# Kernel optimization log

Hardware: AMD Instinct MI355X
Metric: run time of the kernel (lower is better)

## Reference

```python
import jax, jax.numpy as jnp
import numpy as np

B, N, DIM, INTER, HEAD = 2, 2048, 1024, 1024, 16
N_SEG = 4


def setup_inputs() -> dict:
    key = jax.random.key(0)
    k0, k1, k2, k3 = jax.random.split(key, 4)
    features = jax.random.normal(k0, (B, N, DIM), dtype=jnp.float32)
    mask = jax.random.randint(k1, (B, N, N), 0, N_SEG, dtype=jnp.int32)
    W_qkv = jax.random.normal(k2, (DIM, 3 * INTER), dtype=jnp.float32) * 0.02
    W_out = jax.random.normal(k3, (INTER, DIM), dtype=jnp.float32) * 0.02
    return {"features": features, "mask": mask, "W_qkv": W_qkv, "W_out": W_out,
            "n_segments": N_SEG}


def reference(features, mask, W_qkv, W_out, n_segments):
    b, n, dim = features.shape
    h = HEAD
    scale = INTER ** (-0.5)  # NOTE: original scales by inter_dim, not per-head dim
    qkv = features @ W_qkv                              # [b, n, 3*inter]
    q, k, v = jnp.split(qkv, 3, axis=-1)
    q = q.reshape(b, n, h, -1)                          # [b, n, h, d]
    k = k.reshape(b, n, h, -1)
    v = v.reshape(b, n, h, -1)
    alpha = jnp.einsum('bihd,bjhd->bhij', q, k) * scale  # [b, h, n, n]
    exps = jnp.exp(alpha)
    out = jnp.zeros((b, n, h, v.shape[-1]), dtype=features.dtype)
    # loop over fixed small segment-id set; ids absent from mask contribute 0,
    # exactly matching the torch.unique loop in the original.
    for seg in range(n_segments):
        m = (mask == seg)[:, None, :, :]                # [b, 1, n, n] -> broadcast over h
        fe = jnp.where(m, exps, 0.0)
        s = jnp.sum(fe, axis=-1, keepdims=True)
        att = fe / jnp.where(s == 0, 1.0, s)            # masked softmax (no max-shift, faithful)
        out = out + jnp.einsum('bhij,bjhd->bihd', att, v)
    out = out.reshape(b, n, h * v.shape[-1])            # [b, n, inter]
    return out @ W_out                                  # dropout at eval = identity
```

## Files before the change

### kernel.cpp

```cpp
#include <hip/hip_runtime.h>
#include <hip/hip_bf16.h>

#define BB 2
#define NN 2048
#define DIM 1024
#define INTER 1024
#define NHEAD 16
#define HDIM 64
#define NSEG 4
#define QKVW (3 * INTER)

typedef __attribute__((ext_vector_type(8))) short bf16x8;
typedef __attribute__((ext_vector_type(4))) float f32x4;

static __device__ __forceinline__ unsigned short f2bf(float f) {
    __hip_bfloat16 h = __float2bfloat16(f);
    return *reinterpret_cast<unsigned short*>(&h);
}
static __device__ __forceinline__ float bf2f(unsigned short u) {
    unsigned int x = ((unsigned int)u) << 16;
    return __builtin_bit_cast(float, x);
}
static __device__ __forceinline__ unsigned int pack_bf16_rne(float lo, float hi) {
    unsigned int u = __builtin_bit_cast(unsigned int, lo);
    unsigned int v = __builtin_bit_cast(unsigned int, hi);
    u += 0x7FFFu + ((u >> 16) & 1u);
    v += 0x7FFFu + ((v >> 16) & 1u);
    return (u >> 16) | (v & 0xFFFF0000u);
}

__global__ __launch_bounds__(256) void conv_f32_bf16(const float* __restrict__ in,
                                                     unsigned short* __restrict__ out) {
    int i = (blockIdx.x * 256 + threadIdx.x) * 4;
    float4 v = *(const float4*)&in[i];
    ushort4 o = {f2bf(v.x), f2bf(v.y), f2bf(v.z), f2bf(v.w)};
    *(ushort4*)&out[i] = o;
}

__global__ __launch_bounds__(256) void transp_f32_bf16(const float* __restrict__ in,
                                                       unsigned short* __restrict__ out,
                                                       int R, int C) {
    __shared__ float tile[64][65];
    const int r0 = blockIdx.y * 64, c0 = blockIdx.x * 64;
    const int t = threadIdx.x;
#pragma unroll
    for (int it = 0; it < 4; ++it) {
        int r = it * 16 + (t >> 4);
        int c = (t & 15) * 4;
        float4 v = *(const float4*)&in[(size_t)(r0 + r) * C + c0 + c];
        tile[r][c] = v.x; tile[r][c + 1] = v.y; tile[r][c + 2] = v.z; tile[r][c + 3] = v.w;
    }
    __syncthreads();
#pragma unroll
    for (int it = 0; it < 4; ++it) {
        int c = it * 16 + (t >> 4);
        int r = (t & 15) * 4;
        ushort4 o = {f2bf(tile[r][c]), f2bf(tile[r + 1][c]), f2bf(tile[r + 2][c]), f2bf(tile[r + 3][c])};
        *(ushort4*)&out[(size_t)(c0 + c) * R + r0 + r] = o;
    }
}

__global__ __launch_bounds__(256) void transp_split_f32_bf16(const float* __restrict__ in,
                                                             unsigned short* __restrict__ oh,
                                                             unsigned short* __restrict__ ol,
                                                             int R, int C) {
    __shared__ float tile[64][65];
    const int r0 = blockIdx.y * 64, c0 = blockIdx.x * 64;
    const int t = threadIdx.x;
#pragma unroll
    for (int it = 0; it < 4; ++it) {
        int r = it * 16 + (t >> 4);
        int c = (t & 15) * 4;
        float4 v = *(const float4*)&in[(size_t)(r0 + r) * C + c0 + c];
        tile[r][c] = v.x; tile[r][c + 1] = v.y; tile[r][c + 2] = v.z; tile[r][c + 3] = v.w;
    }
    __syncthreads();
#pragma unroll
    for (int it = 0; it < 4; ++it) {
        int c = it * 16 + (t >> 4);
        int r = (t & 15) * 4;
        float v0 = tile[r][c], v1 = tile[r + 1][c], v2 = tile[r + 2][c], v3 = tile[r + 3][c];
        ushort4 hh, ll;
        hh.x = f2bf(v0); ll.x = f2bf(v0 - bf2f(hh.x));
        hh.y = f2bf(v1); ll.y = f2bf(v1 - bf2f(hh.y));
        hh.z = f2bf(v2); ll.z = f2bf(v2 - bf2f(hh.z));
        hh.w = f2bf(v3); ll.w = f2bf(v3 - bf2f(hh.w));
        *(ushort4*)&oh[(size_t)(c0 + c) * R + r0 + r] = hh;
        *(ushort4*)&ol[(size_t)(c0 + c) * R + r0 + r] = ll;
    }
}

#define GBK 32

__global__ __launch_bounds__(256) void gemm_qkv_mfma(
        const unsigned short* __restrict__ A,
        const unsigned short* __restrict__ Bt,
        unsigned short* __restrict__ Cqk,
        unsigned short* __restrict__ Vtg) {
    const int K = 1024;
    __shared__ __align__(16) unsigned short As[128][GBK];
    __shared__ __align__(16) unsigned short Bs[128][GBK];
    const int t = threadIdx.x;
    const int w = t >> 6, lane = t & 63, l15 = lane & 15, quad = lane >> 4;
    const int wr = w >> 1, wc = w & 1;
    const int row0 = blockIdx.y * 128, col0 = blockIdx.x * 128;
    const int lrow = lane >> 2;
    const int lkof = (lane & 3) * 8;

    f32x4 acc[4][4];
#pragma unroll
    for (int i = 0; i < 4; ++i)
#pragma unroll
        for (int j = 0; j < 4; ++j) acc[i][j] = (f32x4){0.f, 0.f, 0.f, 0.f};

    for (int k0 = 0; k0 < K; k0 += GBK) {
#pragma unroll
        for (int c = 0; c < 2; ++c) {
            int rbase = w * 32 + c * 16;
            const unsigned short* ga = A  + (size_t)(row0 + rbase + lrow) * K + k0 + lkof;
            const unsigned short* gb = Bt + (size_t)(col0 + rbase + lrow) * K + k0 + lkof;
            __builtin_amdgcn_global_load_lds(
                (const __attribute__((address_space(1))) void*)ga,
                (__attribute__((address_space(3))) void*)&As[rbase][0], 16, 0, 0);
            __builtin_amdgcn_global_load_lds(
                (const __attribute__((address_space(1))) void*)gb,
                (__attribute__((address_space(3))) void*)&Bs[rbase][0], 16, 0, 0);
        }
        __syncthreads();
        bf16x8 af[4], bfr[4];
#pragma unroll
        for (int i = 0; i < 4; ++i) af[i]  = *(const bf16x8*)&As[wr * 64 + i * 16 + l15][quad * 8];
#pragma unroll
        for (int j = 0; j < 4; ++j) bfr[j] = *(const bf16x8*)&Bs[wc * 64 + j * 16 + l15][quad * 8];
#pragma unroll
        for (int i = 0; i < 4; ++i)
#pragma unroll
            for (int j = 0; j < 4; ++j)
                acc[i][j] = __builtin_amdgcn_mfma_f32_16x16x32_bf16(af[i], bfr[j], acc[i][j], 0, 0, 0);
        __syncthreads();
    }

    if (col0 < 2048) {
        const float qs = (col0 < 1024) ? 0.04508422f : 1.0f;
#pragma unroll
        for (int i = 0; i < 4; ++i)
#pragma unroll
            for (int j = 0; j < 4; ++j)
#pragma unroll
                for (int r = 0; r < 4; ++r) {
                    int row = row0 + wr * 64 + i * 16 + quad * 4 + r;
                    int col = col0 + wc * 64 + j * 16 + l15;
                    Cqk[(size_t)row * 2048 + col] = f2bf(acc[i][j][r] * qs);
                }
    } else {
#pragma unroll
        for (int i = 0; i < 4; ++i)
#pragma unroll
            for (int j = 0; j < 4; ++j) {
                int col = col0 + wc * 64 + j * 16 + l15 - 2048;
                int row = row0 + wr * 64 + i * 16 + quad * 4;
                int bb = row >> 11, n = row & 2047;
                ushort4 o = {f2bf(acc[i][j][0]), f2bf(acc[i][j][1]),
                             f2bf(acc[i][j][2]), f2bf(acc[i][j][3])};
                *(ushort4*)&Vtg[((size_t)bb * INTER + col) * NN + n] = o;
            }
    }
}

__global__ __launch_bounds__(256) void gemm_out_split(
        const unsigned short* __restrict__ Ah,
        const unsigned short* __restrict__ Al,
        const unsigned short* __restrict__ Bh,
        const unsigned short* __restrict__ Bl,
        float* __restrict__ C) {
    const int K = INTER, N = DIM;
    __shared__ __align__(16) unsigned short Ash[128][32];
    __shared__ __align__(16) unsigned short Asl[128][32];
    __shared__ __align__(16) unsigned short Bsh[64][32];
    __shared__ __align__(16) unsigned short Bsl[64][32];
    const int t = threadIdx.x;
    const int w = t >> 6, lane = t & 63, l15 = lane & 15, quad = lane >> 4;
    const int wr = w >> 1, wc = w & 1;
    const int row0 = blockIdx.y * 128, col0 = blockIdx.x * 64;
    const int lrow = lane >> 2, lkof = (lane & 3) * 8;

    f32x4 acc[4][2];
#pragma unroll
    for (int i = 0; i < 4; ++i)
#pragma unroll
        for (int j = 0; j < 2; ++j) acc[i][j] = (f32x4){0.f, 0.f, 0.f, 0.f};

    for (int k0 = 0; k0 < K; k0 += 32) {
#pragma unroll
        for (int c = 0; c < 2; ++c) {
            int rbase = w * 32 + c * 16;
            const unsigned short* gah = Ah + (size_t)(row0 + rbase + lrow) * K + k0 + lkof;
            const unsigned short* gal = Al + (size_t)(row0 + rbase + lrow) * K + k0 + lkof;
            __builtin_amdgcn_global_load_lds(
                (const __attribute__((address_space(1))) void*)gah,
                (__attribute__((address_space(3))) void*)&Ash[rbase][0], 16, 0, 0);
            __builtin_amdgcn_global_load_lds(
                (const __attribute__((address_space(1))) void*)gal,
                (__attribute__((address_space(3))) void*)&Asl[rbase][0], 16, 0, 0);
        }
        {
            int rbase = w * 16;
            const unsigned short* gbh = Bh + (size_t)(col0 + rbase + lrow) * K + k0 + lkof;
            const unsigned short* gbl = Bl + (size_t)(col0 + rbase + lrow) * K + k0 + lkof;
            __builtin_amdgcn_global_load_lds(
                (const __attribute__((address_space(1))) void*)gbh,
                (__attribute__((address_space(3))) void*)&Bsh[rbase][0], 16, 0, 0);
            __builtin_amdgcn_global_load_lds(
                (const __attribute__((address_space(1))) void*)gbl,
                (__attribute__((address_space(3))) void*)&Bsl[rbase][0], 16, 0, 0);
        }
        __syncthreads();
        bf16x8 ah[4], al[4], bh[2], bl[2];
#pragma unroll
        for (int i = 0; i < 4; ++i) {
            ah[i] = *(const bf16x8*)&Ash[wr * 64 + i * 16 + l15][quad * 8];
            al[i] = *(const bf16x8*)&Asl[wr * 64 + i * 16 + l15][quad * 8];
        }
#pragma unroll
        for (int j = 0; j < 2; ++j) {
            bh[j] = *(const bf16x8*)&Bsh[wc * 32 + j * 16 + l15][quad * 8];
            bl[j] = *(const bf16x8*)&Bsl[wc * 32 + j * 16 + l15][quad * 8];
        }
#pragma unroll
        for (int i = 0; i < 4; ++i)
#pragma unroll
            for (int j = 0; j < 2; ++j) {
                acc[i][j] = __builtin_amdgcn_mfma_f32_16x16x32_bf16(ah[i], bh[j], acc[i][j], 0, 0, 0);
                acc[i][j] = __builtin_amdgcn_mfma_f32_16x16x32_bf16(al[i], bh[j], acc[i][j], 0, 0, 0);
                acc[i][j] = __builtin_amdgcn_mfma_f32_16x16x32_bf16(ah[i], bl[j], acc[i][j], 0, 0, 0);
            }
        __syncthreads();
    }
#pragma unroll
    for (int i = 0; i < 4; ++i)
#pragma unroll
        for (int j = 0; j < 2; ++j)
#pragma unroll
            for (int r = 0; r < 4; ++r)
                C[(size_t)(row0 + wr * 64 + i * 16 + quad * 4 + r) * N +
                  col0 + wc * 32 + j * 16 + l15] = acc[i][j][r];
}

__global__ __launch_bounds__(256, 2) void attn_seg_mfma(
        const unsigned short* __restrict__ qk,
        const unsigned short* __restrict__ vtg,
        const int* __restrict__ mask,
        unsigned short* __restrict__ ctxh,
        unsigned short* __restrict__ ctxl) {
    __shared__ __align__(16) unsigned short Ks[2][64 * 64];
    __shared__ __align__(16) unsigned short Vt[2][64 * 64];
    __shared__ __align__(16) unsigned char  Mb[2][64 * 64];
    __shared__ __align__(16) unsigned short El[4][16 * 64];

    const int t    = threadIdx.x;
    const int w    = t >> 6;
    const int lane = t & 63;
    const int l15  = lane & 15;
    const int quad = lane >> 4;
    const int ksw  = (l15 & 7) << 3;
    const int i0   = blockIdx.x * 64;
    const int hh   = blockIdx.y;
    const int b    = blockIdx.z;

    bf16x8 qa0, qa1;
    {
        const unsigned short* qp =
            qk + (size_t)(b * NN + i0 + w * 16 + l15) * 2048 + hh * HDIM + quad * 8;
        qa0 = *(const bf16x8*)qp;
        qa1 = *(const bf16x8*)(qp + 32);
    }

    bf16x8 onesb;
    {
        short ob = (l15 == 0) ? (short)0x3F80 : (short)0;
#pragma unroll
        for (int j = 0; j < 8; ++j) onesb[j] = ob;
    }

    f32x4 acc[NSEG][5];
#pragma unroll
    for (int m = 0; m < NSEG; ++m)
#pragma unroll
        for (int nt = 0; nt < 5; ++nt) acc[m][nt] = (f32x4){0.f, 0.f, 0.f, 0.f};

    auto stage = [&](int bb, int j0) {
#pragma unroll
        for (int it = 0; it < 2; ++it) {
            int id = t + it * 256, key = id >> 3, dc = (id & 7) * 8;
            *(bf16x8*)&Ks[bb][key * 64 + (dc ^ ((key & 7) << 3))] =
                *(const bf16x8*)&qk[(size_t)(b * NN + j0 + key) * 2048 + 1024 + hh * HDIM + dc];
        }
#pragma unroll
        for (int it = 0; it < 2; ++it) {
            int id = t + it * 256, d = id >> 3, c = (id & 7) * 8;
            *(bf16x8*)&Vt[bb][d * 64 + (c ^ ((d & 7) << 3))] =
                *(const bf16x8*)&vtg[((size_t)b * INTER + hh * HDIM + d) * NN + j0 + c];
        }
#pragma unroll
        for (int it = 0; it < 4; ++it) {
            int id = t + it * 256, row = id >> 4, c4 = (id & 15) * 4;
            int4 mv = *(const int4*)&mask[(size_t)(b * NN + i0 + row) * NN + j0 + c4];
            unsigned int p = (unsigned)(mv.x & 3) | ((unsigned)(mv.y & 3) << 8) |
                             ((unsigned)(mv.z & 3) << 16) | ((unsigned)(mv.w & 3) << 24);
            *(unsigned int*)&Mb[bb][row * 64 + c4] = p;
        }
    };

    stage(0, 0);

    for (int jt = 0; jt < NN / 64; ++jt) {
        __syncthreads();
        if (jt + 1 < NN / 64) stage((jt + 1) & 1, (jt + 1) * 64);
        const int bb = jt & 1;

#pragma unroll
        for (int nt = 0; nt < 4; ++nt) {
            f32x4 s = {0.f, 0.f, 0.f, 0.f};
            bf16x8 kb0 = *(const bf16x8*)&Ks[bb][(nt * 16 + l15) * 64 + ((quad * 8) ^ ksw)];
            bf16x8 kb1 = *(const bf16x8*)&Ks[bb][(nt * 16 + l15) * 64 + ((32 + quad * 8) ^ ksw)];
            s = __builtin_amdgcn_mfma_f32_16x16x32_bf16(kb0, qa0, s, 0, 0, 0);
            s = __builtin_amdgcn_mfma_f32_16x16x32_bf16(kb1, qa1, s, 0, 0, 0);
            float e0 = __builtin_amdgcn_exp2f(s[0]);
            float e1 = __builtin_amdgcn_exp2f(s[1]);
            float e2 = __builtin_amdgcn_exp2f(s[2]);
            float e3 = __builtin_amdgcn_exp2f(s[3]);
            uint2 pk;
            pk.x = pack_bf16_rne(e0, e1);
            pk.y = pack_bf16_rne(e2, e3);
            *(uint2*)&El[w][l15 * 64 + ((nt * 16 + quad * 4) ^ ksw)] = pk;
        }

#pragma unroll
        for (int ks = 0; ks < 2; ++ks) {
            union { int4 i; bf16x8 v; } ef;
            ef.i = *(const int4*)&El[w][l15 * 64 + ((ks * 32 + quad * 8) ^ ksw)];
            uint2 sbv = *(const uint2*)&Mb[bb][(w * 16 + l15) * 64 + ks * 32 + quad * 8];
            unsigned int dup[4];
            dup[0] = __builtin_amdgcn_perm(0u, sbv.x, 0x01010000u);
            dup[1] = __builtin_amdgcn_perm(0u, sbv.x, 0x03030202u);
            dup[2] = __builtin_amdgcn_perm(0u, sbv.y, 0x01010000u);
            dup[3] = __builtin_amdgcn_perm(0u, sbv.y, 0x03030202u);
            const unsigned int* ed = (const unsigned int*)&ef.i;
            bf16x8 vb[4];
#pragma unroll
            for (int nt = 0; nt < 4; ++nt)
                vb[nt] = *(const bf16x8*)&Vt[bb][(nt * 16 + l15) * 64 + ((ks * 32 + quad * 8) ^ ksw)];
            __builtin_amdgcn_s_setprio(1);
#pragma unroll
            for (int m = 0; m < NSEG; ++m) {
                const unsigned int Tm = 0xFFu << (8 * m);
                union { int4 i; bf16x8 v; } wm;
#pragma unroll
                for (int d = 0; d < 4; ++d)
                    ((unsigned int*)&wm.i)[d] = ed[d] & __builtin_amdgcn_perm(0u, Tm, dup[d]);
#pragma unroll
                for (int nt = 0; nt < 4; ++nt)
                    acc[m][nt] = __builtin_amdgcn_mfma_f32_16x16x32_bf16(wm.v, vb[nt], acc[m][nt], 0, 0, 0);
                acc[m][4] = __builtin_amdgcn_mfma_f32_16x16x32_bf16(wm.v, onesb, acc[m][4], 0, 0, 0);
            }
            __builtin_amdgcn_s_setprio(0);
        }
    }

    float rres[NSEG][4];
#pragma unroll
    for (int m = 0; m < NSEG; ++m)
#pragma unroll
        for (int r = 0; r < 4; ++r) {
            float sum = __shfl(acc[m][4][r], lane & 48, 64);
            rres[m][r] = (sum > 0.f) ? (1.f / sum) : 0.f;
        }
#pragma unroll
    for (int nt = 0; nt < 4; ++nt)
#pragma unroll
        for (int r = 0; r < 4; ++r) {
            float v = acc[0][nt][r] * rres[0][r] + acc[1][nt][r] * rres[1][r] +
                      acc[2][nt][r] * rres[2][r] + acc[3][nt][r] * rres[3][r];
            size_t idx = (size_t)(b * NN + i0 + w * 16 + quad * 4 + r) * INTER +
                         hh * HDIM + nt * 16 + l15;
            unsigned short uh = f2bf(v);
            ctxh[idx] = uh;
            ctxl[idx] = f2bf(v - bf2f(uh));
        }
}

extern "C" void kernel_launch(void* const* d_in, const int* in_sizes, int n_in,
                              void* d_out, int out_size, void* d_ws, size_t ws_size,
                              hipStream_t stream) {
    const float* features = (const float*)d_in[0];
    const int*   mask     = (const int*)d_in[1];
    const float* W_qkv    = (const float*)d_in[2];
    const float* W_out    = (const float*)d_in[3];
    float* out = (float*)d_out;

    const int M = BB * NN;
    char* ws = (char*)d_ws;
    unsigned short* qk2  = (unsigned short*)ws;
    ws += (size_t)M * 2048 * 2;
    unsigned short* vtg  = (unsigned short*)ws;
    ws += (size_t)BB * INTER * NN * 2;
    unsigned short* ctxh = (unsigned short*)ws;
    ws += (size_t)M * INTER * 2;
    unsigned short* ctxl = (unsigned short*)ws;
    ws += (size_t)M * INTER * 2;
    unsigned short* featb = (unsigned short*)ws;
    ws += (size_t)M * DIM * 2;
    unsigned short* wqt = (unsigned short*)ws;
    unsigned short* woh = wqt;
    unsigned short* wol = wqt + (size_t)DIM * INTER;

    dim3 blk(256);

    conv_f32_bf16<<<dim3((M * DIM) / 1024), blk, 0, stream>>>(features, featb);
    transp_f32_bf16<<<dim3(QKVW / 64, DIM / 64), blk, 0, stream>>>(W_qkv, wqt, DIM, QKVW);

    gemm_qkv_mfma<<<dim3(QKVW / 128, M / 128), blk, 0, stream>>>(featb, wqt, qk2, vtg);

    transp_split_f32_bf16<<<dim3(DIM / 64, INTER / 64), blk, 0, stream>>>(
        W_out, woh, wol, INTER, DIM);

    attn_seg_mfma<<<dim3(NN / 64, NHEAD, BB), blk, 0, stream>>>(qk2, vtg, mask, ctxh, ctxl);

    gemm_out_split<<<dim3(DIM / 64, M / 128), blk, 0, stream>>>(
        ctxh, ctxl, woh, wol, out);
}
```

Baseline: 295.1 us.

## Pre-pack int32 mask to bytes once and streamline attention staging addressing

```diff
diff --git a/kernel.cpp b/kernel.cpp
--- a/kernel.cpp
+++ b/kernel.cpp
@@ -35,6 +35,21 @@
     float4 v = *(const float4*)&in[i];
     ushort4 o = {f2bf(v.x), f2bf(v.y), f2bf(v.z), f2bf(v.w)};
     *(ushort4*)&out[i] = o;
+}
+
+__global__ __launch_bounds__(256) void mask_pack(const int* __restrict__ m,
+                                                 unsigned char* __restrict__ o) {
+    size_t i = (size_t)(blockIdx.x * 256 + threadIdx.x) * 16;
+    int4 a = *(const int4*)&m[i];
+    int4 b = *(const int4*)&m[i + 4];
+    int4 c = *(const int4*)&m[i + 8];
+    int4 d = *(const int4*)&m[i + 12];
+    uint4 p;
+    p.x = (unsigned)(a.x & 3) | ((unsigned)(a.y & 3) << 8) | ((unsigned)(a.z & 3) << 16) | ((unsigned)(a.w & 3) << 24);
+    p.y = (unsigned)(b.x & 3) | ((unsigned)(b.y & 3) << 8) | ((unsigned)(b.z & 3) << 16) | ((unsigned)(b.w & 3) << 24);
+    p.z = (unsigned)(c.x & 3) | ((unsigned)(c.y & 3) << 8) | ((unsigned)(c.z & 3) << 16) | ((unsigned)(c.w & 3) << 24);
+    p.w = (unsigned)(d.x & 3) | ((unsigned)(d.y & 3) << 8) | ((unsigned)(d.z & 3) << 16) | ((unsigned)(d.w & 3) << 24);
+    *(uint4*)&o[i] = p;
 }
 
 __global__ __launch_bounds__(256) void transp_f32_bf16(const float* __restrict__ in,
@@ -249,13 +264,13 @@
 __global__ __launch_bounds__(256, 2) void attn_seg_mfma(
         const unsigned short* __restrict__ qk,
         const unsigned short* __restrict__ vtg,
-        const int* __restrict__ mask,
+        const unsigned char* __restrict__ maskb,
         unsigned short* __restrict__ ctxh,
         unsigned short* __restrict__ ctxl) {
-    __shared__ __align__(16) unsigned short Ks[2][64 * 64];
-    __shared__ __align__(16) unsigned short Vt[2][64 * 64];
-    __shared__ __align__(16) unsigned char  Mb[2][64 * 64];
-    __shared__ __align__(16) unsigned short El[4][16 * 64];
+    __shared__ __align__(16) unsigned short KsL[2 * 4096];
+    __shared__ __align__(16) unsigned short VtL[2 * 4096];
+    __shared__ __align__(16) unsigned char  MbL[2 * 5120];
+    __shared__ __align__(16) unsigned short El4[4 * 1024];
 
     const int t    = threadIdx.x;
     const int w    = t >> 6;
@@ -267,6 +282,28 @@
     const int hh   = blockIdx.y;
     const int b    = blockIdx.z;
 
+    const int c0   = (quad * 8) ^ ksw;
+    const int c1   = (32 + quad * 8) ^ ksw;
+    const int a0   = l15 * 64 + c0;
+    const int a1   = l15 * 64 + c1;
+    const int wEl  = w * 1024;
+    int ew[4];
+#pragma unroll
+    for (int nt = 0; nt < 4; ++nt) ew[nt] = l15 * 64 + ((nt * 16 + quad * 4) ^ ksw);
+    const int ef0 = wEl + l15 * 64 + c0;
+    const int ef1 = wEl + l15 * 64 + c1;
+    const int mrd = (w * 16 + l15) * 80 + quad * 8;
+
+    const int skey = t >> 3, sdc = (t & 7) * 8;
+    const unsigned short* pK0 = qk + (size_t)(b * NN + skey) * 2048 + 1024 + hh * HDIM + sdc;
+    const unsigned short* pK1 = pK0 + (size_t)32 * 2048;
+    const int wK0 = skey * 64 + (sdc ^ ((skey & 7) << 3));
+    const int wK1 = (skey + 32) * 64 + (sdc ^ ((skey & 7) << 3));
+    const unsigned short* pV0 = vtg + ((size_t)b * INTER + hh * HDIM + skey) * NN + sdc;
+    const unsigned short* pV1 = pV0 + (size_t)32 * NN;
+    const unsigned char* pM = maskb + (size_t)(b * NN + i0 + (t >> 2)) * NN + (t & 3) * 16;
+    const int wM = (t >> 2) * 80 + (t & 3) * 16;
+
     bf16x8 qa0, qa1;
     {
         const unsigned short* qp =
@@ -288,41 +325,32 @@
 #pragma unroll
         for (int nt = 0; nt < 5; ++nt) acc[m][nt] = (f32x4){0.f, 0.f, 0.f, 0.f};
 
-    auto stage = [&](int bb, int j0) {
-#pragma unroll
-        for (int it = 0; it < 2; ++it) {
-            int id = t + it * 256, key = id >> 3, dc = (id & 7) * 8;
-            *(bf16x8*)&Ks[bb][key * 64 + (dc ^ ((key & 7) << 3))] =
-                *(const bf16x8*)&qk[(size_t)(b * NN + j0 + key) * 2048 + 1024 + hh * HDIM + dc];
-        }
-#pragma unroll
-        for (int it = 0; it < 2; ++it) {
-            int id = t + it * 256, d = id >> 3, c = (id & 7) * 8;
-            *(bf16x8*)&Vt[bb][d * 64 + (c ^ ((d & 7) << 3))] =
-                *(const bf16x8*)&vtg[((size_t)b * INTER + hh * HDIM + d) * NN + j0 + c];
-        }
-#pragma unroll
-        for (int it = 0; it < 4; ++it) {
-            int id = t + it * 256, row = id >> 4, c4 = (id & 15) * 4;
-            int4 mv = *(const int4*)&mask[(size_t)(b * NN + i0 + row) * NN + j0 + c4];
-            unsigned int p = (unsigned)(mv.x & 3) | ((unsigned)(mv.y & 3) << 8) |
-                             ((unsigned)(mv.z & 3) << 16) | ((unsigned)(mv.w & 3) << 24);
-            *(unsigned int*)&Mb[bb][row * 64 + c4] = p;
-        }
+    auto stage = [&](int bb) {
+        unsigned short* ksb = &KsL[bb << 12];
+        unsigned short* vtb = &VtL[bb << 12];
+        *(bf16x8*)&ksb[wK0] = *(const bf16x8*)pK0;
+        *(bf16x8*)&ksb[wK1] = *(const bf16x8*)pK1;
+        *(bf16x8*)&vtb[wK0 - (skey * 64 - skey * 64)] = *(const bf16x8*)pV0;
+        *(bf16x8*)&vtb[wK1] = *(const bf16x8*)pV1;
+        *(uint4*)&MbL[bb * 5120 + wM] = *(const uint4*)pM;
+        pK0 += (size_t)64 * 2048; pK1 += (size_t)64 * 2048;
+        pV0 += 64; pV1 += 64;
+        pM += 64;
     };
 
-    stage(0, 0);
+    stage(0);
 
     for (int jt = 0; jt < NN / 64; ++jt) {
         __syncthreads();
-        if (jt + 1 < NN / 64) stage((jt + 1) & 1, (jt + 1) * 64);
-        const int bb = jt & 1;
+        if (jt + 1 < NN / 64) stage((jt + 1) & 1);
+        const int bbase = (jt & 1) << 12;
+        const int mbase = (jt & 1) * 5120;
 
 #pragma unroll
         for (int nt = 0; nt < 4; ++nt) {
             f32x4 s = {0.f, 0.f, 0.f, 0.f};
-            bf16x8 kb0 = *(const bf16x8*)&Ks[bb][(nt * 16 + l15) * 64 + ((quad * 8) ^ ksw)];
-            bf16x8 kb1 = *(const bf16x8*)&Ks[bb][(nt * 16 + l15) * 64 + ((32 + quad * 8) ^ ksw)];
+            bf16x8 kb0 = *(const bf16x8*)&KsL[bbase + a0 + nt * 1024];
+            bf16x8 kb1 = *(const bf16x8*)&KsL[bbase + a1 + nt * 1024];
             s = __builtin_amdgcn_mfma_f32_16x16x32_bf16(kb0, qa0, s, 0, 0, 0);
             s = __builtin_amdgcn_mfma_f32_16x16x32_bf16(kb1, qa1, s, 0, 0, 0);
             float e0 = __builtin_amdgcn_exp2f(s[0]);
@@ -332,14 +360,14 @@
             uint2 pk;
             pk.x = pack_bf16_rne(e0, e1);
             pk.y = pack_bf16_rne(e2, e3);
-            *(uint2*)&El[w][l15 * 64 + ((nt * 16 + quad * 4) ^ ksw)] = pk;
+            *(uint2*)&El4[wEl + ew[nt]] = pk;
         }
 
 #pragma unroll
         for (int ks = 0; ks < 2; ++ks) {
             union { int4 i; bf16x8 v; } ef;
-            ef.i = *(const int4*)&El[w][l15 * 64 + ((ks * 32 + quad * 8) ^ ksw)];
-            uint2 sbv = *(const uint2*)&Mb[bb][(w * 16 + l15) * 64 + ks * 32 + quad * 8];
+            ef.i = *(const int4*)&El4[ks ? ef1 : ef0];
+            uint2 sbv = *(const uint2*)&MbL[mbase + mrd + ks * 32];
             unsigned int dup[4];
             dup[0] = __builtin_amdgcn_perm(0u, sbv.x, 0x01010000u);
             dup[1] = __builtin_amdgcn_perm(0u, sbv.x, 0x03030202u);
@@ -349,7 +377,7 @@
             bf16x8 vb[4];
 #pragma unroll
             for (int nt = 0; nt < 4; ++nt)
-                vb[nt] = *(const bf16x8*)&Vt[bb][(nt * 16 + l15) * 64 + ((ks * 32 + quad * 8) ^ ksw)];
+                vb[nt] = *(const bf16x8*)&VtL[bbase + (ks ? a1 : a0) + nt * 1024];
             __builtin_amdgcn_s_setprio(1);
 #pragma unroll
             for (int m = 0; m < NSEG; ++m) {
@@ -411,12 +439,16 @@
     unsigned short* featb = (unsigned short*)ws;
     ws += (size_t)M * DIM * 2;
     unsigned short* wqt = (unsigned short*)ws;
+    ws += (size_t)QKVW * DIM * 2;
+    unsigned char* maskb = (unsigned char*)ws;
+    ws += (size_t)BB * NN * NN;
     unsigned short* woh = wqt;
     unsigned short* wol = wqt + (size_t)DIM * INTER;
 
     dim3 blk(256);
 
     conv_f32_bf16<<<dim3((M * DIM) / 1024), blk, 0, stream>>>(features, featb);
+    mask_pack<<<dim3((BB * NN * NN) / (256 * 16)), blk, 0, stream>>>(mask, maskb);
     transp_f32_bf16<<<dim3(QKVW / 64, DIM / 64), blk, 0, stream>>>(W_qkv, wqt, DIM, QKVW);
 
     gemm_qkv_mfma<<<dim3(QKVW / 128, M / 128), blk, 0, stream>>>(featb, wqt, qk2, vtg);
@@ -424,7 +456,7 @@
     transp_split_f32_bf16<<<dim3(DIM / 64, INTER / 64), blk, 0, stream>>>(
         W_out, woh, wol, INTER, DIM);
 
-    attn_seg_mfma<<<dim3(NN / 64, NHEAD, BB), blk, 0, stream>>>(qk2, vtg, mask, ctxh, ctxl);
+    attn_seg_mfma<<<dim3(NN / 64, NHEAD, BB), blk, 0, stream>>>(qk2, vtg, maskb, ctxh, ctxl);
 
     gemm_out_split<<<dim3(DIM / 64, M / 128), blk, 0, stream>>>(
         ctxh, ctxl, woh, wol, out);
```

Measured after the change: 280.2 us. -5.0%, faster.
